# Optimization experiments

Measured on AMD Instinct MI355X. Metric: run time of the kernel, lower is better.

## Reference

```python
import jax, jax.numpy as jnp
import numpy as np

B, T, V, E, H = 256, 512, 100000, 128, 256


def setup_inputs() -> dict:
    key = jax.random.key(0)
    ks = jax.random.split(key, 16)
    s_e = 1.0 / np.sqrt(H)
    inp = {
        "x": jax.random.randint(ks[0], (B, T), 0, V, dtype=jnp.int32),
        "lengths": jax.random.randint(ks[1], (B,), 1, T + 1, dtype=jnp.int32),
        "embedding": jax.random.normal(ks[2], (V, E), jnp.float32),
        "w_ih_f": jax.random.uniform(ks[3], (3 * H, E), jnp.float32, -s_e, s_e),
        "w_hh_f": jax.random.uniform(ks[4], (3 * H, H), jnp.float32, -s_e, s_e),
        "b_ih_f": jax.random.uniform(ks[5], (3 * H,), jnp.float32, -s_e, s_e),
        "b_hh_f": jax.random.uniform(ks[6], (3 * H,), jnp.float32, -s_e, s_e),
        "w_ih_b": jax.random.uniform(ks[7], (3 * H, E), jnp.float32, -s_e, s_e),
        "w_hh_b": jax.random.uniform(ks[8], (3 * H, H), jnp.float32, -s_e, s_e),
        "b_ih_b": jax.random.uniform(ks[9], (3 * H,), jnp.float32, -s_e, s_e),
        "b_hh_b": jax.random.uniform(ks[10], (3 * H,), jnp.float32, -s_e, s_e),
        "fc1_w": jax.random.uniform(ks[11], (128, 2 * H), jnp.float32, -0.05, 0.05),
        "fc1_b": jnp.zeros((128,), jnp.float32),
        "fc2_w": jax.random.uniform(ks[12], (64, 128), jnp.float32, -0.09, 0.09),
        "fc2_b": jnp.zeros((64,), jnp.float32),
    }
    return inp


def _gru_dir(xp, w_hh, b_hh, lengths, reverse):
    # xp: [T, B, 3H] precomputed input projections; returns final hidden [B, H].
    Tn, Bn, H3 = xp.shape
    Hn = H3 // 3
    ts = jnp.arange(Tn)

    def step(h, inputs):
        xt, t = inputs
        hh = h @ w_hh.T + b_hh
        xr, xz, xn = jnp.split(xt, 3, axis=-1)
        hr, hz, hn = jnp.split(hh, 3, axis=-1)
        r = jax.nn.sigmoid(xr + hr)
        z = jax.nn.sigmoid(xz + hz)
        n = jnp.tanh(xn + r * hn)
        h_new = (1.0 - z) * n + z * h
        # ragged masking: only update state while t < length (packed-sequence semantics)
        h = jnp.where((t < lengths)[:, None], h_new, h)
        return h, None

    h0 = jnp.zeros((Bn, Hn), xp.dtype)
    h_final, _ = jax.lax.scan(step, h0, (xp, ts), reverse=reverse)
    return h_final


def reference(x, lengths, embedding, w_ih_f, w_hh_f, b_ih_f, b_hh_f,
              w_ih_b, w_hh_b, b_ih_b, b_hh_b, fc1_w, fc1_b, fc2_w, fc2_b):
    emb = embedding[x]                     # [B, T, E]
    xt = emb.transpose(1, 0, 2)            # [T, B, E]
    xp_f = xt @ w_ih_f.T + b_ih_f          # [T, B, 3H]
    xp_b = xt @ w_ih_b.T + b_ih_b
    hf = _gru_dir(xp_f, w_hh_f, b_hh_f, lengths, reverse=False)   # h_n forward
    hb = _gru_dir(xp_b, w_hh_b, b_hh_b, lengths, reverse=True)    # h_n backward
    h = jnp.concatenate([hf, hb], axis=1)  # [B, 2H]
    hid = jax.nn.relu(h @ fc1_w.T + fc1_b)
    out = hid @ fc2_w.T + fc2_b            # [B, 64]
    norm = jnp.linalg.norm(out, axis=1, keepdims=True)
    return out / jnp.maximum(norm, 1e-12)
```

## Files before the change

kernel.cpp:

```cpp
#include <hip/hip_runtime.h>
#include <hip/hip_bf16.h>

#define B_ 256
#define T_ 512
#define E_ 128
#define H_ 256

typedef __attribute__((ext_vector_type(8))) short short8;
typedef __attribute__((ext_vector_type(4))) float f32x4;
typedef unsigned short u16;

#define MFMA_BF16(a, b, c) __builtin_amdgcn_mfma_f32_16x16x32_bf16((a), (b), (c), 0, 0, 0)

__device__ __forceinline__ u16 f2bf(float f) {
    union { float f; unsigned int u; } v; v.f = f;
    unsigned int u = v.u;
    unsigned int r = (u + 0x7fffu + ((u >> 16) & 1u)) >> 16;
    return (u16)r;
}
__device__ __forceinline__ float bflo(unsigned int u) {
    union { unsigned int u; float f; } v; v.u = u << 16; return v.f;
}
__device__ __forceinline__ float bfhi(unsigned int u) {
    union { unsigned int u; float f; } v; v.u = u & 0xffff0000u; return v.f;
}
__device__ __forceinline__ f32x4 up2(uint2 p) {
    f32x4 r; r[0] = bflo(p.x); r[1] = bfhi(p.x); r[2] = bflo(p.y); r[3] = bfhi(p.y); return r;
}
__device__ __forceinline__ uint2 pk4(float a, float b, float c, float d) {
    uint2 o;
    asm("v_cvt_pk_bf16_f32 %0, %1, %2" : "=v"(o.x) : "v"(a), "v"(b));
    asm("v_cvt_pk_bf16_f32 %0, %1, %2" : "=v"(o.y) : "v"(c), "v"(d));
    return o;
}
__device__ __forceinline__ float rcp_f(float x) { return __builtin_amdgcn_rcpf(x); }
__device__ __forceinline__ float sigm(float x) { return rcp_f(1.f + __expf(-x)); }

__global__ void f32_to_bf16_kernel(const float* __restrict__ src, u16* __restrict__ dst, int n2) {
    int i = blockIdx.x * blockDim.x + threadIdx.x;
    if (i < n2) {
        float2 v = ((const float2*)src)[i];
        ushort2 o; o.x = f2bf(v.x); o.y = f2bf(v.y);
        ((ushort2*)dst)[i] = o;
    }
}

#define XP_SLOT_U2 49152

__attribute__((amdgpu_flat_work_group_size(512, 512), amdgpu_waves_per_eu(2, 2)))
__global__ void fused_chunk_kernel(const int* __restrict__ x, const float* __restrict__ emb,
                                   const u16* __restrict__ wih, const u16* __restrict__ whh,
                                   const float* __restrict__ bih_f, const float* __restrict__ bhh_f,
                                   const float* __restrict__ bih_b, const float* __restrict__ bhh_b,
                                   const int* __restrict__ lengths,
                                   float* __restrict__ hstate,
                                   u16* __restrict__ xp,
                                   int C, int c, int nchunks) {
    __shared__ u16 hfr[2][4096];
    __shared__ u16 wnA[32768];

    const int tid  = threadIdx.x;
    const int lane = tid & 63;
    const int nl   = lane & 15;
    const int quad = lane >> 4;

    if (blockIdx.x < 32) {
        const int g = c - 1;
        if (g < 0) return;
        const int c0 = g * C;
        const int rg = g & 1;
        const int dir    = blockIdx.x >> 4;
        const int btile  = blockIdx.x & 15;
        const int b_base = btile << 4;
        const int wv     = tid >> 6;

        __builtin_amdgcn_s_setprio(1);

        const u16*   whh_d = whh + (size_t)dir * (768 * 256);
        const float* bhh   = dir ? bhh_b : bhh_f;

        for (int e = tid; e < 4096; e += 512) {
            int wv_e = e >> 9, kt_e = (e >> 6) & 7, ln_e = e & 63;
            const u16* src = whh_d + (size_t)(512 + wv_e * 32 + 16 + (ln_e & 15)) * 256
                           + (ln_e >> 4) * 8 + kt_e * 32;
            *(short8*)&wnA[e * 8] = *(const short8*)src;
        }

        short8 w[5][8];
        {
            const int row[5] = {wv * 32 + nl, wv * 32 + 16 + nl,
                                256 + wv * 32 + nl, 256 + wv * 32 + 16 + nl,
                                512 + wv * 32 + nl};
#pragma unroll
            for (int gh = 0; gh < 5; gh++) {
                const u16* p = whh_d + (size_t)row[gh] * 256 + quad * 8;
#pragma unroll
                for (int kt = 0; kt < 8; kt++) w[gh][kt] = *(const short8*)(p + kt * 32);
            }
        }

        const float4 bnh0 = *(const float4*)(bhh + 512 + wv * 32 + quad * 4);
        const float4 bnh1 = *(const float4*)(bhh + 512 + wv * 32 + 16 + quad * 4);
        const int len = lengths[b_base + nl];

        float hreg[2][4];
        const int o0 = quad * 4, o1 = 16 + quad * 4;
        const int widx0 = (wv * 64 + (o0 >> 3) * 16 + nl) * 8 + (o0 & 7);
        const int widx1 = (wv * 64 + (o1 >> 3) * 16 + nl) * 8 + (o1 & 7);
        if (c0 == 0) {
#pragma unroll
            for (int hh = 0; hh < 2; hh++)
#pragma unroll
                for (int rr = 0; rr < 4; rr++) hreg[hh][rr] = 0.f;
        } else {
            const float* hs = hstate + ((size_t)(dir * 256 + b_base + nl)) * 256 + wv * 32;
            float4 h0 = *(const float4*)(hs + o0);
            float4 h1 = *(const float4*)(hs + o1);
            hreg[0][0] = h0.x; hreg[0][1] = h0.y; hreg[0][2] = h0.z; hreg[0][3] = h0.w;
            hreg[1][0] = h1.x; hreg[1][1] = h1.y; hreg[1][2] = h1.z; hreg[1][3] = h1.w;
        }
        *(uint2*)&hfr[0][widx0] = pk4(hreg[0][0], hreg[0][1], hreg[0][2], hreg[0][3]);
        *(uint2*)&hfr[0][widx1] = pk4(hreg[1][0], hreg[1][1], hreg[1][2], hreg[1][3]);

        const uint2* pg0;
        const uint2* pg1;
        const uint2* pg2;
        {
            size_t base = (((size_t)(rg * 2 * C + dir * C) * 16 + btile) * 48) * 64 + lane;
            pg0 = (const uint2*)xp + base + (0 * 16 + wv * 2) * 64;
            pg1 = (const uint2*)xp + base + (1 * 16 + wv * 2) * 64;
            pg2 = (const uint2*)xp + base + (2 * 16 + wv * 2) * 64;
        }
        uint2 pf0[2], pf1[2], pf2[2];
        pf0[0] = pg0[0]; pf0[1] = pg0[64];
        pf1[0] = pg1[0]; pf1[1] = pg1[64];
        pf2[0] = pg2[0]; pf2[1] = pg2[64];

        __syncthreads();

        for (int ls = 0; ls < C; ls++) {
            const int s = c0 + ls;
            const int t = dir ? (T_ - 1 - s) : s;
            const int cur = ls & 1, nxt = cur ^ 1;

            f32x4 accr[2], accz[2], accn[2], xpn[2];
            accr[0] = up2(pf0[0]); accr[1] = up2(pf0[1]);
            accz[0] = up2(pf1[0]); accz[1] = up2(pf1[1]);
            xpn[0]  = up2(pf2[0]); xpn[1]  = up2(pf2[1]);
            accn[0] = (f32x4){bnh0.x, bnh0.y, bnh0.z, bnh0.w};
            accn[1] = (f32x4){bnh1.x, bnh1.y, bnh1.z, bnh1.w};

            pg0 += XP_SLOT_U2; pg1 += XP_SLOT_U2; pg2 += XP_SLOT_U2;
            pf0[0] = pg0[0]; pf0[1] = pg0[64];
            pf1[0] = pg1[0]; pf1[1] = pg1[64];
            pf2[0] = pg2[0]; pf2[1] = pg2[64];

#pragma unroll
            for (int kt = 0; kt < 8; kt++) {
                short8 hv = *(const short8*)&hfr[cur][(kt * 64 + lane) * 8];
                accr[0] = MFMA_BF16(w[0][kt], hv, accr[0]);
                accr[1] = MFMA_BF16(w[1][kt], hv, accr[1]);
                accz[0] = MFMA_BF16(w[2][kt], hv, accz[0]);
                accz[1] = MFMA_BF16(w[3][kt], hv, accz[1]);
                accn[0] = MFMA_BF16(w[4][kt], hv, accn[0]);
                short8 bn = *(const short8*)&wnA[((wv * 8 + kt) * 64 + lane) * 8];
                accn[1] = MFMA_BF16(bn, hv, accn[1]);
            }

            const bool upd = (t < len);
#pragma unroll
            for (int hh = 0; hh < 2; hh++) {
#pragma unroll
                for (int rr = 0; rr < 4; rr++) {
                    float r = sigm(accr[hh][rr]);
                    float z = sigm(accz[hh][rr]);
                    float npre = xpn[hh][rr] + r * accn[hh][rr];
                    float nn = 1.f - 2.f * rcp_f(1.f + __expf(2.f * npre));
                    float hn = nn + z * (hreg[hh][rr] - nn);
                    if (upd) hreg[hh][rr] = hn;
                }
            }
            *(uint2*)&hfr[nxt][widx0] = pk4(hreg[0][0], hreg[0][1], hreg[0][2], hreg[0][3]);
            *(uint2*)&hfr[nxt][widx1] = pk4(hreg[1][0], hreg[1][1], hreg[1][2], hreg[1][3]);
            __syncthreads();
        }

        float* hs = hstate + ((size_t)(dir * 256 + b_base + nl)) * 256 + wv * 32;
        *(float4*)(hs + o0) = (float4){hreg[0][0], hreg[0][1], hreg[0][2], hreg[0][3]};
        *(float4*)(hs + o1) = (float4){hreg[1][0], hreg[1][1], hreg[1][2], hreg[1][3]};
    } else {
        if (c >= nchunks) return;
        u16 (*A)[136] = (u16 (*)[136])wnA;

        const int mb0 = (int)blockIdx.x - 32;
        const int per_dir = C * 4;
        const int dir = (mb0 >= per_dir) ? 1 : 0;
        const int mb  = mb0 - dir * per_dir;
        const int lt  = mb >> 2;
        const int b0  = (mb & 3) << 6;
        const int c0  = c * C;
        const int t   = dir ? (T_ - 1 - (c0 + lt)) : (c0 + lt);
        const int wv  = tid >> 6;

        const u16*   wih_d = wih + (size_t)dir * (768 * 128);
        const float* bih   = dir ? bih_b : bih_f;
        const float* bhh   = dir ? bhh_b : bhh_f;

        short8 wfrag[6][4];
#pragma unroll
        for (int j = 0; j < 6; j++) {
            int gt = wv * 6 + j;
            const u16* p = wih_d + (size_t)(gt * 16 + nl) * 128 + quad * 8;
#pragma unroll
            for (int kt = 0; kt < 4; kt++) wfrag[j][kt] = *(const short8*)(p + kt * 32);
        }

#pragma unroll
        for (int i = 0; i < 4; i++) {
            int idx = tid + i * 512;
            int r = idx >> 5, cc = idx & 31;
            int tok = x[(b0 + r) * T_ + t];
            float4 v = *(const float4*)(emb + (size_t)tok * E_ + cc * 4);
            *(uint2*)&A[r][cc * 4] = pk4(v.x, v.y, v.z, v.w);
        }
        __syncthreads();

        f32x4 acc[6][4];
#pragma unroll
        for (int j = 0; j < 6; j++)
#pragma unroll
            for (int mi = 0; mi < 4; mi++) acc[j][mi] = (f32x4){0, 0, 0, 0};

#pragma unroll
        for (int kt = 0; kt < 4; kt++) {
            short8 a[4];
#pragma unroll
            for (int mi = 0; mi < 4; mi++)
                a[mi] = *(const short8*)&A[mi * 16 + nl][quad * 8 + kt * 32];
#pragma unroll
            for (int j = 0; j < 6; j++)
#pragma unroll
                for (int mi = 0; mi < 4; mi++)
                    acc[j][mi] = MFMA_BF16(wfrag[j][kt], a[mi], acc[j][mi]);
        }

        const int slot = (c & 1) * 2 * C + dir * C + lt;
#pragma unroll
        for (int j = 0; j < 6; j++) {
            int gt = wv * 6 + j;
            int gate = gt >> 4;
            const float4 bi = *(const float4*)(bih + gt * 16 + quad * 4);
            const float4 bh = *(const float4*)(bhh + gt * 16 + quad * 4);
            float bb[4];
            bb[0] = bi.x + (gate < 2 ? bh.x : 0.f);
            bb[1] = bi.y + (gate < 2 ? bh.y : 0.f);
            bb[2] = bi.z + (gate < 2 ? bh.z : 0.f);
            bb[3] = bi.w + (gate < 2 ? bh.w : 0.f);
#pragma unroll
            for (int mi = 0; mi < 4; mi++) {
                int btile = ((mb & 3) << 2) + mi;
                f32x4 v = acc[j][mi];
                size_t base = (((size_t)slot * 16 + btile) * 48 + gt) * 64 + lane;
                ((uint2*)xp)[base] = pk4(v[0] + bb[0], v[1] + bb[1], v[2] + bb[2], v[3] + bb[3]);
            }
        }
    }
}

__global__ void fc_head_kernel(const float* __restrict__ hstate,
                               const float* __restrict__ fc1w, const float* __restrict__ fc1b,
                               const float* __restrict__ fc2w, const float* __restrict__ fc2b,
                               float* __restrict__ out) {
    int row = blockIdx.x;
    int tid = threadIdx.x;
    __shared__ float hrow[512];
    __shared__ float hid[128];

    {
        int dir = tid >> 6, u = (tid & 63) * 4;
        float4 hv = *(const float4*)(hstate + ((size_t)(dir * 256 + row)) * 256 + u);
        *(float4*)(hrow + tid * 4) = hv;
    }
    __syncthreads();

    float acc = fc1b[tid];
    const float* wrow = fc1w + (size_t)tid * 512;
#pragma unroll 4
    for (int k = 0; k < 512; k += 4) {
        float4 w = *(const float4*)(wrow + k);
        acc += w.x * hrow[k] + w.y * hrow[k + 1] + w.z * hrow[k + 2] + w.w * hrow[k + 3];
    }
    hid[tid] = fmaxf(acc, 0.f);
    __syncthreads();

    if (tid < 64) {
        float a2 = fc2b[tid];
        const float* w2 = fc2w + (size_t)tid * 128;
#pragma unroll 4
        for (int k = 0; k < 128; k += 4) {
            float4 w = *(const float4*)(w2 + k);
            a2 += w.x * hid[k] + w.y * hid[k + 1] + w.z * hid[k + 2] + w.w * hid[k + 3];
        }
        float ss = a2 * a2;
#pragma unroll
        for (int off = 32; off > 0; off >>= 1) ss += __shfl_down(ss, off);
        ss = __shfl(ss, 0);
        float scale = 1.f / fmaxf(sqrtf(ss), 1e-12f);
        out[(size_t)row * 64 + tid] = a2 * scale;
    }
}

#define OFF_WIH  ((size_t)0)
#define OFF_WHH  ((size_t)393216)
#define OFF_HST  ((size_t)(393216 + 786432))
#define OFF_XP   ((size_t)(393216 + 786432 + 524288))
#define SLOT_B   ((size_t)393216)

extern "C" void kernel_launch(void* const* d_in, const int* in_sizes, int n_in,
                              void* d_out, int out_size, void* d_ws, size_t ws_size,
                              hipStream_t stream) {
    const int*   x      = (const int*)d_in[0];
    const int*   lens   = (const int*)d_in[1];
    const float* embedding = (const float*)d_in[2];
    const float* w_ih_f = (const float*)d_in[3];
    const float* w_hh_f = (const float*)d_in[4];
    const float* b_ih_f = (const float*)d_in[5];
    const float* b_hh_f = (const float*)d_in[6];
    const float* w_ih_b = (const float*)d_in[7];
    const float* w_hh_b = (const float*)d_in[8];
    const float* b_ih_b = (const float*)d_in[9];
    const float* b_hh_b = (const float*)d_in[10];
    const float* fc1_w  = (const float*)d_in[11];
    const float* fc1_b  = (const float*)d_in[12];
    const float* fc2_w  = (const float*)d_in[13];
    const float* fc2_b  = (const float*)d_in[14];
    float* out = (float*)d_out;

    char* ws = (char*)d_ws;
    u16*   wih_bf = (u16*)(ws + OFF_WIH);
    u16*   whh_bf = (u16*)(ws + OFF_WHH);
    float* hstate = (float*)(ws + OFF_HST);
    u16*   xp     = (u16*)(ws + OFF_XP);

    int C = 16;
    if      (ws_size >= OFF_XP + (size_t)(4 * 128 + 1) * SLOT_B) C = 128;
    else if (ws_size >= OFF_XP + (size_t)(4 * 64  + 1) * SLOT_B) C = 64;
    else if (ws_size >= OFF_XP + (size_t)(4 * 32  + 1) * SLOT_B) C = 32;

    f32_to_bf16_kernel<<<192, 256, 0, stream>>>(w_ih_f, wih_bf, 49152);
    f32_to_bf16_kernel<<<192, 256, 0, stream>>>(w_ih_b, wih_bf + 98304, 49152);
    f32_to_bf16_kernel<<<384, 256, 0, stream>>>(w_hh_f, whh_bf, 98304);
    f32_to_bf16_kernel<<<384, 256, 0, stream>>>(w_hh_b, whh_bf + 196608, 98304);

    const int nchunks = T_ / C;
    const int grid = 32 + 8 * C;
    for (int c = 0; c <= nchunks; c++) {
        fused_chunk_kernel<<<grid, 512, 0, stream>>>(x, embedding, wih_bf, whh_bf,
                                                     b_ih_f, b_hh_f, b_ih_b, b_hh_b,
                                                     lens, hstate, xp, C, c, nchunks);
    }

    fc_head_kernel<<<256, 128, 0, stream>>>(hstate, fc1_w, fc1_b, fc2_w, fc2_b, out);
}
```

Baseline: 1.077 ms.

## Halve recurrent block to 4 waves, each handling 64 hidden units

The fused chunk kernel drops from 512 to 256 threads per block. Each wave in the recurrent GRU path now covers 64 hidden units instead of 32, keeping the r and z weight fragments in registers and staging all n-gate weights in a doubled LDS buffer. The projection path likewise gives each wave 12 gate tiles instead of 6. The aim is to cut the per-step barrier cost and wave count on the serial recurrence, at the cost of more MFMAs per wave per step, higher register pressure (one wave per EU) and more LDS reads for the n-gate weights.

```diff
diff --git a/kernel.cpp b/kernel.cpp
--- a/kernel.cpp
+++ b/kernel.cpp
@@ -47,7 +47,7 @@
 
 #define XP_SLOT_U2 49152
 
-__attribute__((amdgpu_flat_work_group_size(512, 512), amdgpu_waves_per_eu(2, 2)))
+__attribute__((amdgpu_flat_work_group_size(256, 256), amdgpu_waves_per_eu(1, 1)))
 __global__ void fused_chunk_kernel(const int* __restrict__ x, const float* __restrict__ emb,
                                    const u16* __restrict__ wih, const u16* __restrict__ whh,
                                    const float* __restrict__ bih_f, const float* __restrict__ bhh_f,
@@ -57,7 +57,7 @@
                                    u16* __restrict__ xp,
                                    int C, int c, int nchunks) {
     __shared__ u16 hfr[2][4096];
-    __shared__ u16 wnA[32768];
+    __shared__ u16 wn4[65536];
 
     const int tid  = threadIdx.x;
     const int lane = tid & 63;
@@ -79,62 +79,70 @@
         const u16*   whh_d = whh + (size_t)dir * (768 * 256);
         const float* bhh   = dir ? bhh_b : bhh_f;
 
-        for (int e = tid; e < 4096; e += 512) {
-            int wv_e = e >> 9, kt_e = (e >> 6) & 7, ln_e = e & 63;
-            const u16* src = whh_d + (size_t)(512 + wv_e * 32 + 16 + (ln_e & 15)) * 256
+        for (int e = tid; e < 8192; e += 256) {
+            int su   = e >> 9;
+            int kt_e = (e >> 6) & 7;
+            int ln_e = e & 63;
+            const u16* src = whh_d + (size_t)(512 + su * 16 + (ln_e & 15)) * 256
                            + (ln_e >> 4) * 8 + kt_e * 32;
-            *(short8*)&wnA[e * 8] = *(const short8*)src;
-        }
-
-        short8 w[5][8];
-        {
-            const int row[5] = {wv * 32 + nl, wv * 32 + 16 + nl,
-                                256 + wv * 32 + nl, 256 + wv * 32 + 16 + nl,
-                                512 + wv * 32 + nl};
-#pragma unroll
-            for (int gh = 0; gh < 5; gh++) {
-                const u16* p = whh_d + (size_t)row[gh] * 256 + quad * 8;
-#pragma unroll
-                for (int kt = 0; kt < 8; kt++) w[gh][kt] = *(const short8*)(p + kt * 32);
-            }
-        }
-
-        const float4 bnh0 = *(const float4*)(bhh + 512 + wv * 32 + quad * 4);
-        const float4 bnh1 = *(const float4*)(bhh + 512 + wv * 32 + 16 + quad * 4);
+            *(short8*)&wn4[e * 8] = *(const short8*)src;
+        }
+
+        short8 w[8][8];
+#pragma unroll
+        for (int s = 0; s < 8; s++) {
+            int gate = s >> 2, ut = s & 3;
+            int row = gate * 256 + wv * 64 + ut * 16 + nl;
+            const u16* p = whh_d + (size_t)row * 256 + quad * 8;
+#pragma unroll
+            for (int kt = 0; kt < 8; kt++) w[s][kt] = *(const short8*)(p + kt * 32);
+        }
+
+        float4 bnh[4];
+#pragma unroll
+        for (int ut = 0; ut < 4; ut++)
+            bnh[ut] = *(const float4*)(bhh + 512 + wv * 64 + ut * 16 + quad * 4);
+
         const int len = lengths[b_base + nl];
 
-        float hreg[2][4];
-        const int o0 = quad * 4, o1 = 16 + quad * 4;
-        const int widx0 = (wv * 64 + (o0 >> 3) * 16 + nl) * 8 + (o0 & 7);
-        const int widx1 = (wv * 64 + (o1 >> 3) * 16 + nl) * 8 + (o1 & 7);
+        float hreg[4][4];
+        int widx[4];
+#pragma unroll
+        for (int ut = 0; ut < 4; ut++) {
+            int u = wv * 64 + ut * 16 + quad * 4;
+            widx[ut] = ((u >> 3) * 16 + nl) * 8 + (u & 7);
+        }
+        float* hs = hstate + ((size_t)(dir * 256 + b_base + nl)) * 256 + wv * 64;
         if (c0 == 0) {
 #pragma unroll
-            for (int hh = 0; hh < 2; hh++)
-#pragma unroll
-                for (int rr = 0; rr < 4; rr++) hreg[hh][rr] = 0.f;
+            for (int ut = 0; ut < 4; ut++)
+#pragma unroll
+                for (int rr = 0; rr < 4; rr++) hreg[ut][rr] = 0.f;
         } else {
-            const float* hs = hstate + ((size_t)(dir * 256 + b_base + nl)) * 256 + wv * 32;
-            float4 h0 = *(const float4*)(hs + o0);
-            float4 h1 = *(const float4*)(hs + o1);
-            hreg[0][0] = h0.x; hreg[0][1] = h0.y; hreg[0][2] = h0.z; hreg[0][3] = h0.w;
-            hreg[1][0] = h1.x; hreg[1][1] = h1.y; hreg[1][2] = h1.z; hreg[1][3] = h1.w;
-        }
-        *(uint2*)&hfr[0][widx0] = pk4(hreg[0][0], hreg[0][1], hreg[0][2], hreg[0][3]);
-        *(uint2*)&hfr[0][widx1] = pk4(hreg[1][0], hreg[1][1], hreg[1][2], hreg[1][3]);
-
-        const uint2* pg0;
-        const uint2* pg1;
-        const uint2* pg2;
+#pragma unroll
+            for (int ut = 0; ut < 4; ut++) {
+                float4 h4 = *(const float4*)(hs + ut * 16 + quad * 4);
+                hreg[ut][0] = h4.x; hreg[ut][1] = h4.y; hreg[ut][2] = h4.z; hreg[ut][3] = h4.w;
+            }
+        }
+#pragma unroll
+        for (int ut = 0; ut < 4; ut++)
+            *(uint2*)&hfr[0][widx[ut]] = pk4(hreg[ut][0], hreg[ut][1], hreg[ut][2], hreg[ut][3]);
+
+        const uint2* pgr;
+        const uint2* pgz;
+        const uint2* pgn;
         {
             size_t base = (((size_t)(rg * 2 * C + dir * C) * 16 + btile) * 48) * 64 + lane;
-            pg0 = (const uint2*)xp + base + (0 * 16 + wv * 2) * 64;
-            pg1 = (const uint2*)xp + base + (1 * 16 + wv * 2) * 64;
-            pg2 = (const uint2*)xp + base + (2 * 16 + wv * 2) * 64;
-        }
-        uint2 pf0[2], pf1[2], pf2[2];
-        pf0[0] = pg0[0]; pf0[1] = pg0[64];
-        pf1[0] = pg1[0]; pf1[1] = pg1[64];
-        pf2[0] = pg2[0]; pf2[1] = pg2[64];
+            pgr = (const uint2*)xp + base + (0 * 16 + wv * 4) * 64;
+            pgz = (const uint2*)xp + base + (1 * 16 + wv * 4) * 64;
+            pgn = (const uint2*)xp + base + (2 * 16 + wv * 4) * 64;
+        }
+        uint2 pfr[4], pfz[4], pfn[4];
+#pragma unroll
+        for (int ut = 0; ut < 4; ut++) {
+            pfr[ut] = pgr[ut * 64]; pfz[ut] = pgz[ut * 64]; pfn[ut] = pgn[ut * 64];
+        }
 
         __syncthreads();
 
@@ -143,54 +151,60 @@
             const int t = dir ? (T_ - 1 - s) : s;
             const int cur = ls & 1, nxt = cur ^ 1;
 
-            f32x4 accr[2], accz[2], accn[2], xpn[2];
-            accr[0] = up2(pf0[0]); accr[1] = up2(pf0[1]);
-            accz[0] = up2(pf1[0]); accz[1] = up2(pf1[1]);
-            xpn[0]  = up2(pf2[0]); xpn[1]  = up2(pf2[1]);
-            accn[0] = (f32x4){bnh0.x, bnh0.y, bnh0.z, bnh0.w};
-            accn[1] = (f32x4){bnh1.x, bnh1.y, bnh1.z, bnh1.w};
-
-            pg0 += XP_SLOT_U2; pg1 += XP_SLOT_U2; pg2 += XP_SLOT_U2;
-            pf0[0] = pg0[0]; pf0[1] = pg0[64];
-            pf1[0] = pg1[0]; pf1[1] = pg1[64];
-            pf2[0] = pg2[0]; pf2[1] = pg2[64];
+            f32x4 accr[4], accz[4], accn[4], xpn[4];
+#pragma unroll
+            for (int ut = 0; ut < 4; ut++) {
+                accr[ut] = up2(pfr[ut]);
+                accz[ut] = up2(pfz[ut]);
+                xpn[ut]  = up2(pfn[ut]);
+                accn[ut] = (f32x4){bnh[ut].x, bnh[ut].y, bnh[ut].z, bnh[ut].w};
+            }
+
+            pgr += XP_SLOT_U2; pgz += XP_SLOT_U2; pgn += XP_SLOT_U2;
+#pragma unroll
+            for (int ut = 0; ut < 4; ut++) {
+                pfr[ut] = pgr[ut * 64]; pfz[ut] = pgz[ut * 64]; pfn[ut] = pgn[ut * 64];
+            }
 
 #pragma unroll
             for (int kt = 0; kt < 8; kt++) {
                 short8 hv = *(const short8*)&hfr[cur][(kt * 64 + lane) * 8];
-                accr[0] = MFMA_BF16(w[0][kt], hv, accr[0]);
-                accr[1] = MFMA_BF16(w[1][kt], hv, accr[1]);
-                accz[0] = MFMA_BF16(w[2][kt], hv, accz[0]);
-                accz[1] = MFMA_BF16(w[3][kt], hv, accz[1]);
-                accn[0] = MFMA_BF16(w[4][kt], hv, accn[0]);
-                short8 bn = *(const short8*)&wnA[((wv * 8 + kt) * 64 + lane) * 8];
-                accn[1] = MFMA_BF16(bn, hv, accn[1]);
+#pragma unroll
+                for (int ut = 0; ut < 4; ut++) {
+                    accr[ut] = MFMA_BF16(w[ut][kt],     hv, accr[ut]);
+                    accz[ut] = MFMA_BF16(w[4 + ut][kt], hv, accz[ut]);
+                    short8 bn = *(const short8*)&wn4[(((wv * 4 + ut) * 8 + kt) * 64 + lane) * 8];
+                    accn[ut] = MFMA_BF16(bn, hv, accn[ut]);
+                }
             }
 
             const bool upd = (t < len);
 #pragma unroll
-            for (int hh = 0; hh < 2; hh++) {
+            for (int ut = 0; ut < 4; ut++) {
 #pragma unroll
                 for (int rr = 0; rr < 4; rr++) {
-                    float r = sigm(accr[hh][rr]);
-                    float z = sigm(accz[hh][rr]);
-                    float npre = xpn[hh][rr] + r * accn[hh][rr];
+                    float r = sigm(accr[ut][rr]);
+                    float z = sigm(accz[ut][rr]);
+                    float npre = xpn[ut][rr] + r * accn[ut][rr];
                     float nn = 1.f - 2.f * rcp_f(1.f + __expf(2.f * npre));
-                    float hn = nn + z * (hreg[hh][rr] - nn);
-                    if (upd) hreg[hh][rr] = hn;
+                    float hn = nn + z * (hreg[ut][rr] - nn);
+                    if (upd) hreg[ut][rr] = hn;
                 }
             }
-            *(uint2*)&hfr[nxt][widx0] = pk4(hreg[0][0], hreg[0][1], hreg[0][2], hreg[0][3]);
-            *(uint2*)&hfr[nxt][widx1] = pk4(hreg[1][0], hreg[1][1], hreg[1][2], hreg[1][3]);
+#pragma unroll
+            for (int ut = 0; ut < 4; ut++)
+                *(uint2*)&hfr[nxt][widx[ut]] =
+                    pk4(hreg[ut][0], hreg[ut][1], hreg[ut][2], hreg[ut][3]);
             __syncthreads();
         }
 
-        float* hs = hstate + ((size_t)(dir * 256 + b_base + nl)) * 256 + wv * 32;
-        *(float4*)(hs + o0) = (float4){hreg[0][0], hreg[0][1], hreg[0][2], hreg[0][3]};
-        *(float4*)(hs + o1) = (float4){hreg[1][0], hreg[1][1], hreg[1][2], hreg[1][3]};
+#pragma unroll
+        for (int ut = 0; ut < 4; ut++)
+            *(float4*)(hs + ut * 16 + quad * 4) =
+                (float4){hreg[ut][0], hreg[ut][1], hreg[ut][2], hreg[ut][3]};
     } else {
         if (c >= nchunks) return;
-        u16 (*A)[136] = (u16 (*)[136])wnA;
+        u16 (*A)[136] = (u16 (*)[136])wn4;
 
         const int mb0 = (int)blockIdx.x - 32;
         const int per_dir = C * 4;
@@ -206,18 +220,18 @@
         const float* bih   = dir ? bih_b : bih_f;
         const float* bhh   = dir ? bhh_b : bhh_f;
 
-        short8 wfrag[6][4];
-#pragma unroll
-        for (int j = 0; j < 6; j++) {
-            int gt = wv * 6 + j;
+        short8 wfrag[12][4];
+#pragma unroll
+        for (int j = 0; j < 12; j++) {
+            int gt = wv * 12 + j;
             const u16* p = wih_d + (size_t)(gt * 16 + nl) * 128 + quad * 8;
 #pragma unroll
             for (int kt = 0; kt < 4; kt++) wfrag[j][kt] = *(const short8*)(p + kt * 32);
         }
 
 #pragma unroll
-        for (int i = 0; i < 4; i++) {
-            int idx = tid + i * 512;
+        for (int i = 0; i < 8; i++) {
+            int idx = tid + i * 256;
             int r = idx >> 5, cc = idx & 31;
             int tok = x[(b0 + r) * T_ + t];
             float4 v = *(const float4*)(emb + (size_t)tok * E_ + cc * 4);
@@ -225,9 +239,9 @@
         }
         __syncthreads();
 
-        f32x4 acc[6][4];
-#pragma unroll
-        for (int j = 0; j < 6; j++)
+        f32x4 acc[12][4];
+#pragma unroll
+        for (int j = 0; j < 12; j++)
 #pragma unroll
             for (int mi = 0; mi < 4; mi++) acc[j][mi] = (f32x4){0, 0, 0, 0};
 
@@ -238,7 +252,7 @@
             for (int mi = 0; mi < 4; mi++)
                 a[mi] = *(const short8*)&A[mi * 16 + nl][quad * 8 + kt * 32];
 #pragma unroll
-            for (int j = 0; j < 6; j++)
+            for (int j = 0; j < 12; j++)
 #pragma unroll
                 for (int mi = 0; mi < 4; mi++)
                     acc[j][mi] = MFMA_BF16(wfrag[j][kt], a[mi], acc[j][mi]);
@@ -246,8 +260,8 @@
 
         const int slot = (c & 1) * 2 * C + dir * C + lt;
 #pragma unroll
-        for (int j = 0; j < 6; j++) {
-            int gt = wv * 6 + j;
+        for (int j = 0; j < 12; j++) {
+            int gt = wv * 12 + j;
             int gate = gt >> 4;
             const float4 bi = *(const float4*)(bih + gt * 16 + quad * 4);
             const float4 bh = *(const float4*)(bhh + gt * 16 + quad * 4);
@@ -355,7 +369,7 @@
     const int nchunks = T_ / C;
     const int grid = 32 + 8 * C;
     for (int c = 0; c <= nchunks; c++) {
-        fused_chunk_kernel<<<grid, 512, 0, stream>>>(x, embedding, wih_bf, whh_bf,
+        fused_chunk_kernel<<<grid, 256, 0, stream>>>(x, embedding, wih_bf, whh_bf,
                                                      b_ih_f, b_hh_f, b_ih_b, b_hh_b,
                                                      lens, hstate, xp, C, c, nchunks);
     }
```

New measurement: 1.712 ms. 1.59x slower.
